# Kernel optimization log

Measured on AMD Instinct MI355X. Metric: run time of the kernel, lower is better.

Reference implementation:

```python
import jax, jax.numpy as jnp
import numpy as np

EPS = 1e-8  # F.cosine_similarity default eps
THRESHOLD = 0.5
NUM_PROTOTYPES = 64
W_DIV_ZP = 1.0
W_DIV_PZ = 1.0
W_DIV_PP = 1.0
W_NUM = 1.0
W_CLUSTER = 1.0
W_SEP = 1.0  # NOTE: original forward applies this weight to cluster_loss (upstream bug), replicated here


def setup_inputs() -> dict:
    key = jax.random.key(0)
    k1, k2, k3, k4, k5 = jax.random.split(key, 5)
    N, IN_DIM, P, D = 4096, 768, NUM_PROTOTYPES, 256
    x = jax.random.normal(k1, (N, IN_DIM), dtype=jnp.float32)
    labels = jax.random.randint(k2, (N,), 0, 2, dtype=jnp.int64)
    # nn.Linear(input_dim, prototype_dim): W stored as [D, IN] in torch; use [IN, D] for x @ W
    bound = 1.0 / np.sqrt(IN_DIM)
    W = jax.random.uniform(k3, (IN_DIM, D), minval=-bound, maxval=bound, dtype=jnp.float32)
    b = jax.random.uniform(k4, (D,), minval=-bound, maxval=bound, dtype=jnp.float32)
    prototypes = jax.random.normal(k5, (P, D), dtype=jnp.float32)
    return {"x": x, "labels": labels, "W": W, "b": b, "prototypes": prototypes}


def _cdist(a, b):
    # Euclidean pairwise distances [Na, Nb]
    d2 = (jnp.sum(a * a, -1)[:, None] + jnp.sum(b * b, -1)[None, :]
          - 2.0 * (a @ b.T))
    return jnp.sqrt(jnp.maximum(d2, 0.0))


def _forward(x, labels, W, b, prototypes):
    P = prototypes.shape[0]
    P_pos = P // 2
    z = x @ W + b  # [N, D]

    zn = z / jnp.maximum(jnp.linalg.norm(z, axis=-1, keepdims=True), EPS)
    pn = prototypes / jnp.maximum(jnp.linalg.norm(prototypes, axis=-1, keepdims=True), EPS)
    cos = zn @ pn.T  # [N, P] cosine similarities

    token_sequences = cos[:, :, None] * prototypes[None, :, :]  # [N, P, D]

    dist = _cdist(z, prototypes)  # [N, P]

    # diversity_loss_z_p: nearest sample per prototype
    ni = jnp.argmin(dist, axis=0)  # [P]
    l_zp = jnp.mean(jnp.linalg.norm(z[ni] - prototypes, axis=-1))

    # diversity_loss_p_z: nearest prototype per sample (intended semantics)
    nj = jnp.argmin(dist, axis=1)  # [N]
    l_pz = jnp.mean(jnp.linalg.norm(z - prototypes[nj], axis=-1))

    # diversity_loss_p_p: mean pairwise prototype distance excluding diagonal
    pp = _cdist(prototypes, prototypes)
    off = 1.0 - jnp.eye(P, dtype=pp.dtype)
    l_pp = jnp.sum(pp * off) / (P * (P - 1))

    # loss_num_prototypes: penalize samples similar to > P/4 prototypes
    num_sim = jnp.sum((cos > THRESHOLD).astype(jnp.float32), axis=1)
    l_num = jnp.sum((num_sim > P / 4).astype(jnp.float32))

    # cluster_loss: 1 - max similarity to own-class prototypes, mean over all samples
    max_pos = jnp.max(cos[:, :P_pos], axis=1)
    max_neg = jnp.max(cos[:, P_pos:], axis=1)
    d_cl = jnp.where(labels == 1, 1.0 - max_pos, 1.0 - max_neg)
    l_cluster = jnp.mean(d_cl)

    loss = (W_DIV_ZP * l_zp + W_DIV_PZ * l_pz + W_DIV_PP * l_pp
            + W_NUM * l_num + W_CLUSTER * l_cluster + W_SEP * l_cluster)
    return token_sequences, loss


def reference(x, labels, W, b, prototypes):
    return _forward(x, labels, W, b, prototypes)
```

## Files before the change

kernel.cpp:

```cpp
#include <hip/hip_runtime.h>
#include <hip/hip_bf16.h>

#define NS 4096
#define IND 768
#define PP 64
#define DD 256
#define EPSF 1e-8f

__global__ void k_init(unsigned int* __restrict__ minu, float* __restrict__ accum) {
    int t = threadIdx.x;
    if (t < PP) minu[t] = 0x7F800000u;
    if (t < 4) accum[t] = 0.0f;
}

__global__ __launch_bounds__(256) void k_gemm(const float* __restrict__ x,
                                              const float* __restrict__ W,
                                              const float* __restrict__ bias,
                                              float* __restrict__ z) {
    __shared__ float As[16][68];
    __shared__ float Bs[16][68];
    int tid = threadIdx.x;
    int tx = tid & 15, ty = tid >> 4;
    int m0 = blockIdx.x * 64, n0 = blockIdx.y * 64;
    float c[4][4] = {};
    for (int k0 = 0; k0 < IND; k0 += 16) {
        {
            int k = tid & 15;
            int mb = tid >> 4;
#pragma unroll
            for (int r = 0; r < 4; ++r) {
                int m = mb + r * 16;
                As[k][m] = x[(m0 + m) * IND + k0 + k];
            }
            int n = tid & 63;
            int kb = tid >> 6;
#pragma unroll
            for (int r = 0; r < 4; ++r) {
                int k2 = kb + r * 4;
                Bs[k2][n] = W[(k0 + k2) * DD + n0 + n];
            }
        }
        __syncthreads();
#pragma unroll
        for (int k = 0; k < 16; ++k) {
            float a[4], bb[4];
#pragma unroll
            for (int i = 0; i < 4; ++i) a[i] = As[k][ty * 4 + i];
#pragma unroll
            for (int j = 0; j < 4; ++j) bb[j] = Bs[k][tx * 4 + j];
#pragma unroll
            for (int i = 0; i < 4; ++i)
#pragma unroll
                for (int j = 0; j < 4; ++j) c[i][j] += a[i] * bb[j];
        }
        __syncthreads();
    }
#pragma unroll
    for (int i = 0; i < 4; ++i) {
        int m = m0 + ty * 4 + i;
#pragma unroll
        for (int j = 0; j < 4; ++j) {
            int n = n0 + tx * 4 + j;
            z[m * DD + n] = c[i][j] + bias[n];
        }
    }
}

__global__ void k_znorm(const float* __restrict__ z, float* __restrict__ znorm) {
    int wave = threadIdx.x >> 6;
    int lane = threadIdx.x & 63;
    int n = blockIdx.x * 4 + wave;
    const float* row = z + n * DD;
    float s = 0.f;
#pragma unroll
    for (int d = lane; d < DD; d += 64) { float v = row[d]; s += v * v; }
#pragma unroll
    for (int o = 1; o < 64; o <<= 1) s += __shfl_xor(s, o);
    if (lane == 0) znorm[n] = sqrtf(s);
}

__global__ void k_proto(const float* __restrict__ protos, float* __restrict__ pnorm,
                        float* __restrict__ accum) {
    int p = blockIdx.x;
    int q = threadIdx.x;
    float s = 0.f;
    for (int d = q; d < DD; d += 64) { float v = protos[p * DD + d]; s += v * v; }
    float t = s;
#pragma unroll
    for (int o = 1; o < 64; o <<= 1) t += __shfl_xor(t, o);
    if (q == 0) pnorm[p] = sqrtf(t);

    float s2 = 0.f;
    for (int d = 0; d < DD; ++d) {
        float diff = protos[p * DD + d] - protos[q * DD + d];
        s2 += diff * diff;
    }
    float dd = (q == p) ? 0.f : sqrtf(s2);
#pragma unroll
    for (int o = 1; o < 64; o <<= 1) dd += __shfl_xor(dd, o);
    if (q == 0) atomicAdd(&accum[3], dd);
}

__global__ __launch_bounds__(256) void k_cos(const float* __restrict__ z,
                                             const float* __restrict__ znorm,
                                             const float* __restrict__ protos,
                                             const float* __restrict__ pnorm,
                                             const int* __restrict__ labels,
                                             float* __restrict__ cosout,
                                             unsigned int* __restrict__ minu,
                                             float* __restrict__ accum) {
    __shared__ float protoT[PP * DD];
    int tid = threadIdx.x;
    for (int idx = tid; idx < PP * DD; idx += 256) {
        int p = idx >> 8, d = idx & 255;
        protoT[d * 64 + (p ^ (d & 31))] = protos[idx];
    }
    __syncthreads();

    int wave = tid >> 6, lane = tid & 63;
    int p = lane;
    float pn = pnorm[p];
    float pn2 = pn * pn;
    float regmin = 3.4e38f;
    float s_pz = 0.f, s_cl = 0.f, s_num = 0.f;

    for (int it = 0; it < 4; ++it) {
        int n = blockIdx.x * 16 + it * 4 + wave;
        const float4* z4 = (const float4*)(z + n * DD);
        float dot = 0.f;
#pragma unroll 16
        for (int d4 = 0; d4 < 64; ++d4) {
            float4 zv = z4[d4];
            int d = d4 * 4;
            dot += zv.x * protoT[(d + 0) * 64 + (p ^ ((d + 0) & 31))];
            dot += zv.y * protoT[(d + 1) * 64 + (p ^ ((d + 1) & 31))];
            dot += zv.z * protoT[(d + 2) * 64 + (p ^ ((d + 2) & 31))];
            dot += zv.w * protoT[(d + 3) * 64 + (p ^ ((d + 3) & 31))];
        }
        float zn = znorm[n];
        float cosv = dot / (fmaxf(zn, EPSF) * fmaxf(pn, EPSF));
        float d2 = zn * zn + pn2 - 2.f * dot;
        float dist = sqrtf(fmaxf(d2, 0.f));
        cosout[n * PP + p] = cosv;

        regmin = fminf(regmin, dist);

        unsigned long long bal = __ballot(cosv > 0.5f);
        int cnt = __popcll(bal);

        float mind = dist;
#pragma unroll
        for (int o = 1; o < 64; o <<= 1) mind = fminf(mind, __shfl_xor(mind, o));
        float mx = cosv;
#pragma unroll
        for (int o = 1; o < 32; o <<= 1) mx = fmaxf(mx, __shfl_xor(mx, o));
        float max_pos = __shfl(mx, 0);
        float max_neg = __shfl(mx, 32);

        if (lane == 0) {
            float dcl = (labels[n] == 1) ? (1.f - max_pos) : (1.f - max_neg);
            s_pz += mind;
            s_cl += dcl;
            if (cnt > 16) s_num += 1.f;
        }
    }
    atomicMin(&minu[p], __float_as_uint(regmin));
    if (lane == 0) {
        atomicAdd(&accum[0], s_pz);
        atomicAdd(&accum[1], s_cl);
        atomicAdd(&accum[2], s_num);
    }
}

__global__ __launch_bounds__(256) void k_write(const float* __restrict__ cosv,
                                               const float* __restrict__ protos,
                                               float* __restrict__ out) {
    int g = blockIdx.x * 256 + threadIdx.x;
    int d4 = g & 63;
    int row = g >> 6;
    int p = row & 63;
    float c = cosv[row];
    float4 v = ((const float4*)protos)[p * 64 + d4];
    float4 r;
    r.x = c * v.x; r.y = c * v.y; r.z = c * v.z; r.w = c * v.w;
    ((float4*)out)[g] = r;
}

__global__ void k_final(const unsigned int* __restrict__ minu,
                        const float* __restrict__ accum,
                        float* __restrict__ out, int out_last) {
    int lane = threadIdx.x;
    float d = __uint_as_float(minu[lane]);
#pragma unroll
    for (int o = 1; o < 64; o <<= 1) d += __shfl_xor(d, o);
    if (lane == 0) {
        float l_zp = d / (float)PP;
        float l_pz = accum[0] / (float)NS;
        float l_cl = accum[1] / (float)NS;
        float l_num = accum[2];
        float l_pp = accum[3] / (float)(PP * (PP - 1));
        out[out_last] = l_zp + l_pz + l_pp + l_num + 2.f * l_cl;
    }
}

extern "C" void kernel_launch(void* const* d_in, const int* in_sizes, int n_in,
                              void* d_out, int out_size, void* d_ws, size_t ws_size,
                              hipStream_t stream) {
    const float* x      = (const float*)d_in[0];
    const int*   labels = (const int*)d_in[1];
    const float* W      = (const float*)d_in[2];
    const float* bias   = (const float*)d_in[3];
    const float* protos = (const float*)d_in[4];
    float* out = (float*)d_out;
    float* ws = (float*)d_ws;

    float* z       = ws;
    float* cosbuf  = ws + 1048576;
    float* znorm   = ws + 1048576 + 262144;
    float* pnorm   = znorm + 4096;
    unsigned int* minu = (unsigned int*)(pnorm + 64);
    float* accum   = (float*)(minu + 64);

    k_init<<<1, 64, 0, stream>>>(minu, accum);
    dim3 ggrid(64, 4);
    k_gemm<<<ggrid, 256, 0, stream>>>(x, W, bias, z);
    k_znorm<<<1024, 256, 0, stream>>>(z, znorm);
    k_proto<<<64, 64, 0, stream>>>(protos, pnorm, accum);
    k_cos<<<256, 256, 0, stream>>>(z, znorm, protos, pnorm, labels, cosbuf, minu, accum);
    k_write<<<65536, 256, 0, stream>>>(cosbuf, protos, out);
    k_final<<<1, 64, 0, stream>>>(minu, accum, out, out_size - 1);
}
```

Measured before the change: 398.7 us.

## Split-K GEMM, fuse norm/bias into cosine kernel, and write token sequences in-kernel

The GEMM is split into two K halves to double the block count, and its partial sums go to two buffers. The cosine kernel combines the halves, adds the bias, computes row norms, and computes dots for four rows per wave from LDS. It then writes the [N,P,D] token sequences directly, dropping the separate write kernel, the cos buffer and the znorm kernel. Init is folded into k_proto and the atomic for the pp sum is replaced by per-prototype stores, which reduces launches. The risk is that the large 256 MB output write now comes from only 256 blocks, which may cap store bandwidth compared with the 65536-block write kernel.

Measured after the change: 368.0 us. 1.08x faster.

```diff
diff --git a/kernel.cpp b/kernel.cpp
--- a/kernel.cpp
+++ b/kernel.cpp
@@ -6,80 +6,10 @@
 #define PP 64
 #define DD 256
 #define EPSF 1e-8f
-
-__global__ void k_init(unsigned int* __restrict__ minu, float* __restrict__ accum) {
-    int t = threadIdx.x;
-    if (t < PP) minu[t] = 0x7F800000u;
-    if (t < 4) accum[t] = 0.0f;
-}
-
-__global__ __launch_bounds__(256) void k_gemm(const float* __restrict__ x,
-                                              const float* __restrict__ W,
-                                              const float* __restrict__ bias,
-                                              float* __restrict__ z) {
-    __shared__ float As[16][68];
-    __shared__ float Bs[16][68];
-    int tid = threadIdx.x;
-    int tx = tid & 15, ty = tid >> 4;
-    int m0 = blockIdx.x * 64, n0 = blockIdx.y * 64;
-    float c[4][4] = {};
-    for (int k0 = 0; k0 < IND; k0 += 16) {
-        {
-            int k = tid & 15;
-            int mb = tid >> 4;
-#pragma unroll
-            for (int r = 0; r < 4; ++r) {
-                int m = mb + r * 16;
-                As[k][m] = x[(m0 + m) * IND + k0 + k];
-            }
-            int n = tid & 63;
-            int kb = tid >> 6;
-#pragma unroll
-            for (int r = 0; r < 4; ++r) {
-                int k2 = kb + r * 4;
-                Bs[k2][n] = W[(k0 + k2) * DD + n0 + n];
-            }
-        }
-        __syncthreads();
-#pragma unroll
-        for (int k = 0; k < 16; ++k) {
-            float a[4], bb[4];
-#pragma unroll
-            for (int i = 0; i < 4; ++i) a[i] = As[k][ty * 4 + i];
-#pragma unroll
-            for (int j = 0; j < 4; ++j) bb[j] = Bs[k][tx * 4 + j];
-#pragma unroll
-            for (int i = 0; i < 4; ++i)
-#pragma unroll
-                for (int j = 0; j < 4; ++j) c[i][j] += a[i] * bb[j];
-        }
-        __syncthreads();
-    }
-#pragma unroll
-    for (int i = 0; i < 4; ++i) {
-        int m = m0 + ty * 4 + i;
-#pragma unroll
-        for (int j = 0; j < 4; ++j) {
-            int n = n0 + tx * 4 + j;
-            z[m * DD + n] = c[i][j] + bias[n];
-        }
-    }
-}
-
-__global__ void k_znorm(const float* __restrict__ z, float* __restrict__ znorm) {
-    int wave = threadIdx.x >> 6;
-    int lane = threadIdx.x & 63;
-    int n = blockIdx.x * 4 + wave;
-    const float* row = z + n * DD;
-    float s = 0.f;
-#pragma unroll
-    for (int d = lane; d < DD; d += 64) { float v = row[d]; s += v * v; }
-#pragma unroll
-    for (int o = 1; o < 64; o <<= 1) s += __shfl_xor(s, o);
-    if (lane == 0) znorm[n] = sqrtf(s);
-}
+#define KHALF 384
 
 __global__ void k_proto(const float* __restrict__ protos, float* __restrict__ pnorm,
+                        float* __restrict__ ppsum, unsigned int* __restrict__ minu,
                         float* __restrict__ accum) {
     int p = blockIdx.x;
     int q = threadIdx.x;
@@ -98,65 +28,149 @@
     float dd = (q == p) ? 0.f : sqrtf(s2);
 #pragma unroll
     for (int o = 1; o < 64; o <<= 1) dd += __shfl_xor(dd, o);
-    if (q == 0) atomicAdd(&accum[3], dd);
-}
-
-__global__ __launch_bounds__(256) void k_cos(const float* __restrict__ z,
-                                             const float* __restrict__ znorm,
-                                             const float* __restrict__ protos,
-                                             const float* __restrict__ pnorm,
-                                             const int* __restrict__ labels,
-                                             float* __restrict__ cosout,
-                                             unsigned int* __restrict__ minu,
-                                             float* __restrict__ accum) {
+    if (q == 0) {
+        ppsum[p] = dd;
+        minu[p] = 0xFFFFFFFFu;
+        if (p == 0) { accum[0] = 0.f; accum[1] = 0.f; accum[2] = 0.f; }
+    }
+}
+
+__global__ __launch_bounds__(256) void k_gemm(const float* __restrict__ x,
+                                              const float* __restrict__ W,
+                                              float* __restrict__ z0,
+                                              float* __restrict__ z1) {
+    __shared__ float As[16][68];
+    __shared__ float Bs[16][68];
+    int tid = threadIdx.x;
+    int tx = tid & 15, ty = tid >> 4;
+    int m0 = blockIdx.x * 64, n0 = blockIdx.y * 64;
+    int kbase = blockIdx.z * KHALF;
+    float* __restrict__ zout = blockIdx.z ? z1 : z0;
+    float c[4][4] = {};
+    for (int k0 = 0; k0 < KHALF; k0 += 16) {
+        {
+            int k = tid & 15;
+            int mb = tid >> 4;
+#pragma unroll
+            for (int r = 0; r < 4; ++r) {
+                int m = mb + r * 16;
+                As[k][m] = x[(m0 + m) * IND + kbase + k0 + k];
+            }
+            int n = tid & 63;
+            int kb = tid >> 6;
+#pragma unroll
+            for (int r = 0; r < 4; ++r) {
+                int k2 = kb + r * 4;
+                Bs[k2][n] = W[(kbase + k0 + k2) * DD + n0 + n];
+            }
+        }
+        __syncthreads();
+#pragma unroll
+        for (int k = 0; k < 16; ++k) {
+            float a[4], bb[4];
+#pragma unroll
+            for (int i = 0; i < 4; ++i) a[i] = As[k][ty * 4 + i];
+#pragma unroll
+            for (int j = 0; j < 4; ++j) bb[j] = Bs[k][tx * 4 + j];
+#pragma unroll
+            for (int i = 0; i < 4; ++i)
+#pragma unroll
+                for (int j = 0; j < 4; ++j) c[i][j] += a[i] * bb[j];
+        }
+        __syncthreads();
+    }
+#pragma unroll
+    for (int i = 0; i < 4; ++i) {
+        int m = m0 + ty * 4 + i;
+#pragma unroll
+        for (int j = 0; j < 4; ++j) zout[m * DD + n0 + tx * 4 + j] = c[i][j];
+    }
+}
+
+__global__ __launch_bounds__(256) void k_cosw(const float* __restrict__ z0,
+                                              const float* __restrict__ z1,
+                                              const float* __restrict__ bias,
+                                              const float* __restrict__ protos,
+                                              const float* __restrict__ pnorm,
+                                              const int* __restrict__ labels,
+                                              float* __restrict__ out,
+                                              unsigned int* __restrict__ minu,
+                                              float* __restrict__ accum) {
     __shared__ float protoT[PP * DD];
+    __shared__ __align__(16) float rowbuf[4][4][DD];
     int tid = threadIdx.x;
     for (int idx = tid; idx < PP * DD; idx += 256) {
         int p = idx >> 8, d = idx & 255;
         protoT[d * 64 + (p ^ (d & 31))] = protos[idx];
     }
-    __syncthreads();
-
-    int wave = tid >> 6, lane = tid & 63;
+
+    int w = tid >> 6, lane = tid & 63;
     int p = lane;
     float pn = pnorm[p];
     float pn2 = pn * pn;
+    float4 b4 = ((const float4*)bias)[lane];
+    int nbase = blockIdx.x * 16 + w * 4;
+
+    float zn[4];
+#pragma unroll
+    for (int s = 0; s < 4; ++s) {
+        int n = nbase + s;
+        float4 a = ((const float4*)z0)[n * 64 + lane];
+        float4 c = ((const float4*)z1)[n * 64 + lane];
+        float4 r;
+        r.x = a.x + c.x + b4.x; r.y = a.y + c.y + b4.y;
+        r.z = a.z + c.z + b4.z; r.w = a.w + c.w + b4.w;
+        float ss = r.x * r.x + r.y * r.y + r.z * r.z + r.w * r.w;
+#pragma unroll
+        for (int o = 1; o < 64; o <<= 1) ss += __shfl_xor(ss, o);
+        zn[s] = sqrtf(ss);
+        ((float4*)rowbuf[w][s])[lane] = r;
+    }
+    __syncthreads();
+
+    float dot0 = 0.f, dot1 = 0.f, dot2 = 0.f, dot3 = 0.f;
+#pragma unroll 8
+    for (int d4 = 0; d4 < 64; ++d4) {
+        float4 r0 = ((const float4*)rowbuf[w][0])[d4];
+        float4 r1 = ((const float4*)rowbuf[w][1])[d4];
+        float4 r2 = ((const float4*)rowbuf[w][2])[d4];
+        float4 r3 = ((const float4*)rowbuf[w][3])[d4];
+        int d = d4 * 4;
+        float p0 = protoT[(d + 0) * 64 + (p ^ ((d + 0) & 31))];
+        float p1 = protoT[(d + 1) * 64 + (p ^ ((d + 1) & 31))];
+        float p2 = protoT[(d + 2) * 64 + (p ^ ((d + 2) & 31))];
+        float p3 = protoT[(d + 3) * 64 + (p ^ ((d + 3) & 31))];
+        dot0 += r0.x * p0 + r0.y * p1 + r0.z * p2 + r0.w * p3;
+        dot1 += r1.x * p0 + r1.y * p1 + r1.z * p2 + r1.w * p3;
+        dot2 += r2.x * p0 + r2.y * p1 + r2.z * p2 + r2.w * p3;
+        dot3 += r3.x * p0 + r3.y * p1 + r3.z * p2 + r3.w * p3;
+    }
+    float dots[4] = {dot0, dot1, dot2, dot3};
+
+    float cosv[4];
     float regmin = 3.4e38f;
     float s_pz = 0.f, s_cl = 0.f, s_num = 0.f;
-
-    for (int it = 0; it < 4; ++it) {
-        int n = blockIdx.x * 16 + it * 4 + wave;
-        const float4* z4 = (const float4*)(z + n * DD);
-        float dot = 0.f;
-#pragma unroll 16
-        for (int d4 = 0; d4 < 64; ++d4) {
-            float4 zv = z4[d4];
-            int d = d4 * 4;
-            dot += zv.x * protoT[(d + 0) * 64 + (p ^ ((d + 0) & 31))];
-            dot += zv.y * protoT[(d + 1) * 64 + (p ^ ((d + 1) & 31))];
-            dot += zv.z * protoT[(d + 2) * 64 + (p ^ ((d + 2) & 31))];
-            dot += zv.w * protoT[(d + 3) * 64 + (p ^ ((d + 3) & 31))];
-        }
-        float zn = znorm[n];
-        float cosv = dot / (fmaxf(zn, EPSF) * fmaxf(pn, EPSF));
-        float d2 = zn * zn + pn2 - 2.f * dot;
+#pragma unroll
+    for (int s = 0; s < 4; ++s) {
+        int n = nbase + s;
+        float dot = dots[s];
+        float c = dot / (fmaxf(zn[s], EPSF) * fmaxf(pn, EPSF));
+        cosv[s] = c;
+        float d2 = zn[s] * zn[s] + pn2 - 2.f * dot;
         float dist = sqrtf(fmaxf(d2, 0.f));
-        cosout[n * PP + p] = cosv;
-
         regmin = fminf(regmin, dist);
 
-        unsigned long long bal = __ballot(cosv > 0.5f);
+        unsigned long long bal = __ballot(c > 0.5f);
         int cnt = __popcll(bal);
 
         float mind = dist;
 #pragma unroll
         for (int o = 1; o < 64; o <<= 1) mind = fminf(mind, __shfl_xor(mind, o));
-        float mx = cosv;
+        float mx = c;
 #pragma unroll
         for (int o = 1; o < 32; o <<= 1) mx = fmaxf(mx, __shfl_xor(mx, o));
         float max_pos = __shfl(mx, 0);
         float max_neg = __shfl(mx, 32);
-
         if (lane == 0) {
             float dcl = (labels[n] == 1) ? (1.f - max_pos) : (1.f - max_neg);
             s_pz += mind;
@@ -170,36 +184,38 @@
         atomicAdd(&accum[1], s_cl);
         atomicAdd(&accum[2], s_num);
     }
-}
-
-__global__ __launch_bounds__(256) void k_write(const float* __restrict__ cosv,
-                                               const float* __restrict__ protos,
-                                               float* __restrict__ out) {
-    int g = blockIdx.x * 256 + threadIdx.x;
-    int d4 = g & 63;
-    int row = g >> 6;
-    int p = row & 63;
-    float c = cosv[row];
-    float4 v = ((const float4*)protos)[p * 64 + d4];
-    float4 r;
-    r.x = c * v.x; r.y = c * v.y; r.z = c * v.z; r.w = c * v.w;
-    ((float4*)out)[g] = r;
+
+    const float4* pr4 = (const float4*)protos;
+#pragma unroll
+    for (int s = 0; s < 4; ++s) {
+        int n = nbase + s;
+        float4* o4 = (float4*)out + (size_t)n * 4096 + lane;
+        float cv = cosv[s];
+#pragma unroll 4
+        for (int pp = 0; pp < 64; ++pp) {
+            float c = __shfl(cv, pp);
+            float4 v = pr4[pp * 64 + lane];
+            float4 r;
+            r.x = c * v.x; r.y = c * v.y; r.z = c * v.z; r.w = c * v.w;
+            o4[pp * 64] = r;
+        }
+    }
 }
 
 __global__ void k_final(const unsigned int* __restrict__ minu,
+                        const float* __restrict__ ppsum,
                         const float* __restrict__ accum,
                         float* __restrict__ out, int out_last) {
     int lane = threadIdx.x;
-    float d = __uint_as_float(minu[lane]);
-#pragma unroll
-    for (int o = 1; o < 64; o <<= 1) d += __shfl_xor(d, o);
+    float v = __uint_as_float(minu[lane]) / (float)PP
+            + ppsum[lane] / (float)(PP * (PP - 1));
+#pragma unroll
+    for (int o = 1; o < 64; o <<= 1) v += __shfl_xor(v, o);
     if (lane == 0) {
-        float l_zp = d / (float)PP;
         float l_pz = accum[0] / (float)NS;
         float l_cl = accum[1] / (float)NS;
         float l_num = accum[2];
-        float l_pp = accum[3] / (float)(PP * (PP - 1));
-        out[out_last] = l_zp + l_pz + l_pp + l_num + 2.f * l_cl;
+        out[out_last] = v + l_pz + l_num + 2.f * l_cl;
     }
 }
 
@@ -214,19 +230,16 @@
     float* out = (float*)d_out;
     float* ws = (float*)d_ws;
 
-    float* z       = ws;
-    float* cosbuf  = ws + 1048576;
-    float* znorm   = ws + 1048576 + 262144;
-    float* pnorm   = znorm + 4096;
-    unsigned int* minu = (unsigned int*)(pnorm + 64);
-    float* accum   = (float*)(minu + 64);
-
-    k_init<<<1, 64, 0, stream>>>(minu, accum);
-    dim3 ggrid(64, 4);
-    k_gemm<<<ggrid, 256, 0, stream>>>(x, W, bias, z);
-    k_znorm<<<1024, 256, 0, stream>>>(z, znorm);
-    k_proto<<<64, 64, 0, stream>>>(protos, pnorm, accum);
-    k_cos<<<256, 256, 0, stream>>>(z, znorm, protos, pnorm, labels, cosbuf, minu, accum);
-    k_write<<<65536, 256, 0, stream>>>(cosbuf, protos, out);
-    k_final<<<1, 64, 0, stream>>>(minu, accum, out, out_size - 1);
-}
+    float* z0    = ws;
+    float* z1    = ws + 1048576;
+    float* pnorm = ws + 2097152;
+    float* ppsum = pnorm + 64;
+    unsigned int* minu = (unsigned int*)(ppsum + 64);
+    float* accum = (float*)(minu + 64);
+
+    k_proto<<<64, 64, 0, stream>>>(protos, pnorm, ppsum, minu, accum);
+    dim3 ggrid(64, 4, 2);
+    k_gemm<<<ggrid, 256, 0, stream>>>(x, W, z0, z1);
+    k_cosw<<<256, 256, 0, stream>>>(z0, z1, bias, protos, pnorm, labels, out, minu, accum);
+    k_final<<<1, 64, 0, stream>>>(minu, ppsum, accum, out, out_size - 1);
+}
```
